# Optimization experiments

Hardware: AMD Instinct MI355X
Metric: run time of the kernel (lower is better)

The kernel has to match this reference:

```python
import jax, jax.numpy as jnp
import numpy as np

TEMPERATURE = 0.07
BASE_TEMPERATURE = 0.07


def _pairwise_euclid(x):
    # torch.cdist(x, x, p=2), with safe sqrt (zero grad at zero distance)
    sq = jnp.sum(x * x, axis=1)
    d2 = sq[:, None] + sq[None, :] - 2.0 * (x @ x.T)
    d2 = jnp.maximum(d2, 0.0)
    safe = jnp.where(d2 > 0.0, d2, 1.0)
    return jnp.where(d2 > 0.0, jnp.sqrt(safe), 0.0)


def setup_inputs() -> dict:
    key = jax.random.key(0)
    k1, k2 = jax.random.split(key)
    features = jax.random.normal(k1, (1024, 2, 512), dtype=jnp.float32)
    labels = jax.random.uniform(k2, (1024,), dtype=jnp.float32)
    return {"features": features, "labels": labels}


def reference(features, labels):
    B, V, D = features.shape
    N = B * V
    # torch.cat(torch.unbind(features, dim=1), dim=0): views stacked -> [N, D]
    cf = features.transpose(1, 0, 2).reshape(N, D)
    lab = jnp.tile(labels, V)  # label of row i is labels[i % B]

    dist = _pairwise_euclid(cf)              # [N, N]
    logits = -dist / TEMPERATURE
    eye = jnp.eye(N, dtype=logits.dtype)
    w = jnp.exp(logits) * (1.0 - eye)        # exp(logits) with l == i excluded

    dis = jnp.abs(lab[:, None] - lab[None, :])  # |y_i - y_j|, symmetric

    # negative[i, j] = sum_{l != i, |y_l - y_i| >= |y_i - y_j|} exp(logits[i, l])
    # computed per-row via sort + suffix cumsum + searchsorted (O(N^2 log N))
    order = jnp.argsort(dis, axis=1)
    sorted_d = jnp.take_along_axis(dis, order, axis=1)
    sorted_w = jnp.take_along_axis(w, order, axis=1)
    suffix = jnp.flip(jnp.cumsum(jnp.flip(sorted_w, axis=1), axis=1), axis=1)
    suffix = jnp.concatenate([suffix, jnp.zeros((N, 1), suffix.dtype)], axis=1)  # [N, N+1]
    # side='left': counts entries strictly < d, so suffix[idx] sums all >= d (ties incl.)
    idx = jax.vmap(lambda sd, d: jnp.searchsorted(sd, d, side='left'))(sorted_d, dis)
    negative = jnp.take_along_axis(suffix, idx, axis=1)
    negative = negative * (1.0 - eye) + eye  # diag set to 1 (log -> 0)

    logits_z = logits * (1.0 - eye)          # logits[i, i] = 0
    log_prob = logits_z - jnp.log(negative)
    mean_log_prob_pos = jnp.sum(log_prob, axis=1) / (N - 1)
    loss = -(TEMPERATURE / BASE_TEMPERATURE) * jnp.mean(mean_log_prob_pos)
    return loss
```

## Files before the change

### kernel.cpp

```cpp
#include <hip/hip_runtime.h>
#include <math.h>


#define NN 2048
#define BB 1024
#define DD 512
#define NT 256
#define NEGINF (-INFINITY)
#define CS 64.0f

typedef short s16x8 __attribute__((ext_vector_type(8)));
typedef float f32x4 __attribute__((ext_vector_type(4)));

__device__ __forceinline__ const float* cf_row(const float* F, int i) {
    return F + ((size_t)(i & (BB - 1)) * 2 + (size_t)(i >> 10)) * DD;
}

__device__ __forceinline__ unsigned bf_rne(float x) {
    const unsigned u = __float_as_uint(x);
    return (u + 0x7FFFu + ((u >> 16) & 1u)) >> 16;
}
__device__ __forceinline__ float bf_val(unsigned h) {
    return __uint_as_float(h << 16);
}

__global__ __launch_bounds__(512) void prep_sort_kernel(const float* __restrict__ F,
                                                        const float* __restrict__ labels,
                                                        ushort* __restrict__ Ahi,
                                                        ushort* __restrict__ Alo,
                                                        float* __restrict__ sq,
                                                        float* __restrict__ slab,
                                                        int* __restrict__ sj) {
    __shared__ float lab[BB];
    const int blk = blockIdx.x;
    const int t = threadIdx.x;

    if (blk < 256) {
        const int lane = t & 63;
        const int w = t >> 6;
        const int i = blk * 8 + w;
        const float* src = cf_row(F, i);
        const float4 v0 = reinterpret_cast<const float4*>(src)[lane];
        const float4 v1 = reinterpret_cast<const float4*>(src)[lane + 64];
        float ss = v0.x * v0.x + v0.y * v0.y + v0.z * v0.z + v0.w * v0.w
                 + v1.x * v1.x + v1.y * v1.y + v1.z * v1.z + v1.w * v1.w;
        #pragma unroll
        for (int st = 32; st > 0; st >>= 1) ss += __shfl_down(ss, st);
        if (lane == 0) sq[i] = ss;

        const float a[8] = {v0.x, v0.y, v0.z, v0.w, v1.x, v1.y, v1.z, v1.w};
        ushort h[8], l[8];
        #pragma unroll
        for (int e = 0; e < 8; ++e) {
            const unsigned hb = bf_rne(a[e]);
            h[e] = (ushort)hb;
            l[e] = (ushort)bf_rne(a[e] - bf_val(hb));
        }
        const size_t base = (size_t)i * DD;
        *reinterpret_cast<ushort4*>(&Ahi[base + lane * 4])       = make_ushort4(h[0], h[1], h[2], h[3]);
        *reinterpret_cast<ushort4*>(&Ahi[base + 256 + lane * 4]) = make_ushort4(h[4], h[5], h[6], h[7]);
        *reinterpret_cast<ushort4*>(&Alo[base + lane * 4])       = make_ushort4(l[0], l[1], l[2], l[3]);
        *reinterpret_cast<ushort4*>(&Alo[base + 256 + lane * 4]) = make_ushort4(l[4], l[5], l[6], l[7]);
    } else {
        lab[t] = labels[t];
        lab[t + 512] = labels[t + 512];
        __syncthreads();
        const int e = (blk - 256) * 512 + t;
        const float li = lab[e];
        int rank = 0;
        const float4* l4 = reinterpret_cast<const float4*>(lab);
        #pragma unroll 4
        for (int j = 0; j < BB / 4; ++j) {
            const float4 v = l4[j];
            const int j0 = j * 4;
            rank += (v.x < li) || (v.x == li && (j0 + 0) < e);
            rank += (v.y < li) || (v.y == li && (j0 + 1) < e);
            rank += (v.z < li) || (v.z == li && (j0 + 2) < e);
            rank += (v.w < li) || (v.w == li && (j0 + 3) < e);
        }
        slab[2 * rank]     = li;
        slab[2 * rank + 1] = li;
        sj[2 * rank]     = e;
        sj[2 * rank + 1] = e + BB;
    }
}

#define TM 64
#define TN 64
#define TK 32
__global__ __launch_bounds__(256) void gemm_dist_kernel(const ushort* __restrict__ Ahi,
                                                        const ushort* __restrict__ Alo,
                                                        const float* __restrict__ sq,
                                                        const int* __restrict__ sj,
                                                        float* __restrict__ distp) {
    __shared__ ushort Ah[4][TM][8];
    __shared__ ushort Al[4][TM][8];
    __shared__ ushort Bh[4][TN][8];
    __shared__ ushort Bl[4][TN][8];
    __shared__ int   sjcA[TM];
    __shared__ int   sjcB[TN];
    __shared__ float sqA[TM];
    __shared__ float sqB[TN];

    const int t = threadIdx.x;
    const int lane = t & 63;
    const int w = t >> 6;

    const int id = blockIdx.x;
    int by = (int)((__fsqrt_rn(8.0f * (float)id + 1.0f) - 1.0f) * 0.5f);
    while ((by + 1) * (by + 2) / 2 <= id) ++by;
    while (by * (by + 1) / 2 > id) --by;
    const int bx = id - by * (by + 1) / 2;
    const int row0 = by * TM;
    const int col0 = bx * TN;
    const bool below = (bx < by);

    if (t < TM) {
        const int s = sj[row0 + t];
        sjcA[t] = s; sqA[t] = sq[s];
    } else if (t < TM + TN) {
        const int u = t - TM;
        const int s = sj[col0 + u];
        sjcB[u] = s; sqB[u] = sq[s];
    }
    __syncthreads();
    const int rr = t >> 2;
    const int cq = t & 3;
    const size_t gA = (size_t)sjcA[rr] * DD + cq * 8;
    const size_t gB = (size_t)sjcB[rr] * DD + cq * 8;

    f32x4 acc[4] = {};
    const int m = lane & 15;
    const int q = lane >> 4;

    for (int kt = 0; kt < DD / TK; ++kt) {
        __syncthreads();
        const size_t ko = (size_t)kt * TK;
        *reinterpret_cast<int4*>(&Ah[cq][rr][0]) = *reinterpret_cast<const int4*>(&Ahi[gA + ko]);
        *reinterpret_cast<int4*>(&Al[cq][rr][0]) = *reinterpret_cast<const int4*>(&Alo[gA + ko]);
        *reinterpret_cast<int4*>(&Bh[cq][rr][0]) = *reinterpret_cast<const int4*>(&Ahi[gB + ko]);
        *reinterpret_cast<int4*>(&Bl[cq][rr][0]) = *reinterpret_cast<const int4*>(&Alo[gB + ko]);
        __syncthreads();

        const s16x8 fah = *reinterpret_cast<const s16x8*>(&Ah[q][w * 16 + m][0]);
        const s16x8 fal = *reinterpret_cast<const s16x8*>(&Al[q][w * 16 + m][0]);
        #pragma unroll
        for (int nt = 0; nt < 4; ++nt) {
            const s16x8 fbh = *reinterpret_cast<const s16x8*>(&Bh[q][nt * 16 + m][0]);
            const s16x8 fbl = *reinterpret_cast<const s16x8*>(&Bl[q][nt * 16 + m][0]);
            acc[nt] = __builtin_amdgcn_mfma_f32_16x16x32_bf16(fah, fbh, acc[nt], 0, 0, 0);
            acc[nt] = __builtin_amdgcn_mfma_f32_16x16x32_bf16(fah, fbl, acc[nt], 0, 0, 0);
            acc[nt] = __builtin_amdgcn_mfma_f32_16x16x32_bf16(fal, fbh, acc[nt], 0, 0, 0);
        }
    }

    const int lr0 = w * 16 + q * 4;
    #pragma unroll
    for (int nt = 0; nt < 4; ++nt) {
        const int lc = nt * 16 + m;
        float o[4];
        #pragma unroll
        for (int r = 0; r < 4; ++r) {
            const float d2 = sqA[lr0 + r] + sqB[lc] - 2.0f * acc[nt][r];
            o[r] = (d2 > 0.f) ? sqrtf(d2) : 0.f;
        }
        #pragma unroll
        for (int r = 0; r < 4; ++r)
            distp[(size_t)(row0 + lr0 + r) * NN + col0 + lc] = o[r];
        if (below) {
            const float4 o4 = make_float4(o[0], o[1], o[2], o[3]);
            *reinterpret_cast<float4*>(&distp[(size_t)(col0 + lc) * NN + row0 + lr0]) = o4;
        }
    }
}

__device__ __forceinline__ int bs_right(const float* key, float d, int lo, int hi) {
    while (lo < hi) {
        const int mid = (lo + hi) >> 1;
        if (key[mid] >= d) hi = mid; else lo = mid + 1;
    }
    return lo;
}
__device__ __forceinline__ int bs_left(const float* key, float d, int lo, int hi) {
    while (lo < hi) {
        const int mid = (lo + hi) >> 1;
        if (key[mid] < d) hi = mid; else lo = mid + 1;
    }
    return lo;
}

__global__ __launch_bounds__(512) void row_kernel(const float* __restrict__ distp,
                                                  const float* __restrict__ slab,
                                                  double* __restrict__ rowval) {
    __shared__ float key[NN];
    __shared__ float Pf[NN];
    __shared__ float Sf[NN + 1];
    __shared__ float wmxA[8], wmxB[8], wps[8], wss[8];
    __shared__ double wDA[8], wLA[8], wDB[8], wLB[8];

    const int pr = blockIdx.x;
    const int rA = 2 * pr, rB = 2 * pr + 1;
    const int t = threadIdx.x;
    const int lane = t & 63;
    const int w = t >> 6;
    const float x = slab[rA];
    const float negInvT = -1.0f / 0.07f;
    const float* drowA = &distp[(size_t)rA * NN];
    const float* drowB = &distp[(size_t)rB * NN];

    {
        const float4 l4 = reinterpret_cast<const float4*>(slab)[t];
        key[t * 4 + 0] = fabsf(l4.x - x);
        key[t * 4 + 1] = fabsf(l4.y - x);
        key[t * 4 + 2] = fabsf(l4.z - x);
        key[t * 4 + 3] = fabsf(l4.w - x);
    }
    const int cb = t * 4;
    float vA[4], vB[4];
    double dsumA = 0.0, dsumB = 0.0;
    float mxA = NEGINF, mxB = NEGINF;
    {
        const float4 a4 = reinterpret_cast<const float4*>(drowA)[t];
        const float4 b4 = reinterpret_cast<const float4*>(drowB)[t];
        const float av[4] = {a4.x, a4.y, a4.z, a4.w};
        const float bv[4] = {b4.x, b4.y, b4.z, b4.w};
        #pragma unroll
        for (int c = 0; c < 4; ++c) {
            const int pc = cb + c;
            if (pc == rA) vA[c] = NEGINF;
            else { const float vv = av[c] * negInvT; vA[c] = vv; mxA = fmaxf(mxA, vv); dsumA += (double)av[c]; }
            if (pc == rB) vB[c] = NEGINF;
            else { const float vv = bv[c] * negInvT; vB[c] = vv; mxB = fmaxf(mxB, vv); dsumB += (double)bv[c]; }
        }
    }
    #pragma unroll
    for (int st = 32; st > 0; st >>= 1) {
        mxA = fmaxf(mxA, __shfl_down(mxA, st));
        mxB = fmaxf(mxB, __shfl_down(mxB, st));
    }
    if (lane == 0) { wmxA[w] = mxA; wmxB[w] = mxB; }
    __syncthreads();
    const float MA = fmaxf(fmaxf(fmaxf(wmxA[0], wmxA[1]), fmaxf(wmxA[2], wmxA[3])),
                           fmaxf(fmaxf(wmxA[4], wmxA[5]), fmaxf(wmxA[6], wmxA[7])));
    const float MB = fmaxf(fmaxf(fmaxf(wmxB[0], wmxB[1]), fmaxf(wmxB[2], wmxB[3])),
                           fmaxf(fmaxf(wmxB[4], wmxB[5]), fmaxf(wmxB[6], wmxB[7])));

    int L8[4], R8[4];
    const int a = cb, b = cb + 3;
    {
        const int le = (rA - 1 < b) ? rA - 1 : b;
        if (a <= le) {
            const float da = key[a];
            const int Ra = bs_right(key, da, rA, NN);
            int Rl = Ra;
            if (le > a) Rl = bs_right(key, key[le], rA, Ra);
            for (int p = a; p <= le; ++p) {
                const float d = key[p];
                int R;
                if (p == a) R = Ra;
                else if (p == le) R = Rl;
                else R = bs_right(key, d, Rl, Ra);
                int L = p + 1;
                while (L < rA && key[L] == d) ++L;
                L8[p - a] = L; R8[p - a] = R;
            }
        }
        const int rs = (rA + 1 > a) ? rA + 1 : a;
        if (rs <= b) {
            const float dr = key[rs];
            const int Lr = bs_left(key, dr, 0, rA);
            int Lb = Lr;
            if (b > rs) Lb = bs_left(key, key[b], 0, Lr);
            for (int p = rs; p <= b; ++p) {
                const float d = key[p];
                int L;
                if (p == rs) L = Lr;
                else if (p == b) L = Lb;
                else L = bs_left(key, d, Lb, Lr);
                int R = p;
                while (R > rA && key[R - 1] == d) --R;
                L8[p - a] = L; R8[p - a] = R;
            }
        }
        if (rA >= a && rA <= b) { L8[rA - a] = rA; R8[rA - a] = rA; }
    }

    double lnsumA = 0.0;
    {
        float e8[4];
        #pragma unroll
        for (int jj = 0; jj < 4; ++jj) e8[jj] = __expf(vA[jj] - MA + CS);
        {
            float run = 0.f, ex[4];
            #pragma unroll
            for (int jj = 0; jj < 4; ++jj) { ex[jj] = run; run += e8[jj]; }
            float inc = run;
            #pragma unroll
            for (int st = 1; st < 64; st <<= 1) {
                const float nm = __shfl_up(inc, st);
                if (lane >= st) inc += nm;
            }
            float xofs = __shfl_up(inc, 1);
            if (lane == 0) xofs = 0.f;
            if (lane == 63) wps[w] = inc;
            __syncthreads();
            #pragma unroll
            for (int ww = 0; ww < 7; ++ww)
                if (ww < w) xofs += wps[ww];
            #pragma unroll
            for (int jj = 0; jj < 4; ++jj) Pf[cb + jj] = ex[jj] + xofs;
        }
        {
            float run = 0.f, sx[4];
            #pragma unroll
            for (int jj = 3; jj >= 0; --jj) { run += e8[jj]; sx[jj] = run; }
            float inc = run;
            #pragma unroll
            for (int st = 1; st < 64; st <<= 1) {
                const float nm = __shfl_down(inc, st);
                if (lane + st < 64) inc += nm;
            }
            float xofs = __shfl_down(inc, 1);
            if (lane == 63) xofs = 0.f;
            if (lane == 0) wss[w] = inc;
            __syncthreads();
            #pragma unroll
            for (int ww = 1; ww < 8; ++ww)
                if (ww > w) xofs += wss[ww];
            #pragma unroll
            for (int jj = 0; jj < 4; ++jj) Sf[cb + jj] = sx[jj] + xofs;
            if (t == 0) Sf[NN] = 0.f;
        }
        __syncthreads();
        const float MBA = MA - CS;
        #pragma unroll
        for (int jj = 0; jj < 4; ++jj) {
            const int p = cb + jj;
            if (p == rA) continue;
            const float s = fmaxf(Pf[L8[jj]] + Sf[R8[jj]], 1e-38f);
            lnsumA += (double)(MBA + __logf(s));
        }
    }
    __syncthreads();

    double lnsumB = 0.0;
    {
        float e8[4];
        #pragma unroll
        for (int jj = 0; jj < 4; ++jj) e8[jj] = __expf(vB[jj] - MB + CS);
        {
            float run = 0.f, ex[4];
            #pragma unroll
            for (int jj = 0; jj < 4; ++jj) { ex[jj] = run; run += e8[jj]; }
            float inc = run;
            #pragma unroll
            for (int st = 1; st < 64; st <<= 1) {
                const float nm = __shfl_up(inc, st);
                if (lane >= st) inc += nm;
            }
            float xofs = __shfl_up(inc, 1);
            if (lane == 0) xofs = 0.f;
            if (lane == 63) wps[w] = inc;
            __syncthreads();
            #pragma unroll
            for (int ww = 0; ww < 7; ++ww)
                if (ww < w) xofs += wps[ww];
            #pragma unroll
            for (int jj = 0; jj < 4; ++jj) Pf[cb + jj] = ex[jj] + xofs;
        }
        {
            float run = 0.f, sx[4];
            #pragma unroll
            for (int jj = 3; jj >= 0; --jj) { run += e8[jj]; sx[jj] = run; }
            float inc = run;
            #pragma unroll
            for (int st = 1; st < 64; st <<= 1) {
                const float nm = __shfl_down(inc, st);
                if (lane + st < 64) inc += nm;
            }
            float xofs = __shfl_down(inc, 1);
            if (lane == 63) xofs = 0.f;
            if (lane == 0) wss[w] = inc;
            __syncthreads();
            #pragma unroll
            for (int ww = 1; ww < 8; ++ww)
                if (ww > w) xofs += wss[ww];
            #pragma unroll
            for (int jj = 0; jj < 4; ++jj) Sf[cb + jj] = sx[jj] + xofs;
            if (t == 0) Sf[NN] = 0.f;
        }
        __syncthreads();
        const float MBB = MB - CS;
        #pragma unroll
        for (int jj = 0; jj < 4; ++jj) {
            const int p = cb + jj;
            if (p == rB) continue;
            const float s = fmaxf(Pf[L8[jj]] + Sf[R8[jj]], 1e-38f);
            lnsumB += (double)(MBB + __logf(s));
        }
    }

    #pragma unroll
    for (int st = 32; st > 0; st >>= 1) {
        dsumA  += __shfl_down(dsumA, st);
        lnsumA += __shfl_down(lnsumA, st);
        dsumB  += __shfl_down(dsumB, st);
        lnsumB += __shfl_down(lnsumB, st);
    }
    if (lane == 0) { wDA[w] = dsumA; wLA[w] = lnsumA; wDB[w] = dsumB; wLB[w] = lnsumB; }
    __syncthreads();
    if (t == 0) {
        double dA = 0.0, lA = 0.0, dB = 0.0, lB = 0.0;
        #pragma unroll
        for (int ww = 0; ww < 8; ++ww) { dA += wDA[ww]; lA += wLA[ww]; dB += wDB[ww]; lB += wLB[ww]; }
        rowval[rA] = (-dA / 0.07) - lA;
        rowval[rB] = (-dB / 0.07) - lB;
    }
}

__global__ __launch_bounds__(256) void finalize_kernel(const double* __restrict__ rowval,
                                                       float* __restrict__ out) {
    __shared__ double red[NT];
    const int t = threadIdx.x;
    double s = 0.0;
    for (int j = t; j < NN; j += NT) s += rowval[j];
    red[t] = s;
    __syncthreads();
    for (int ofs = NT / 2; ofs > 0; ofs >>= 1) {
        if (t < ofs) red[t] += red[t + ofs];
        __syncthreads();
    }
    if (t == 0) {
        out[0] = (float)(-red[0] / ((double)NN * (double)(NN - 1)));
    }
}

extern "C" void kernel_launch(void* const* d_in, const int* in_sizes, int n_in,
                              void* d_out, int out_size, void* d_ws, size_t ws_size,
                              hipStream_t stream) {
    const float* features = (const float*)d_in[0];
    const float* labels   = (const float*)d_in[1];
    float* out = (float*)d_out;

    char* ws = (char*)d_ws;
    size_t off = 0;
    float*  sq     = (float*) (ws + off); off += NN * sizeof(float);
    float*  slab   = (float*) (ws + off); off += NN * sizeof(float);
    int*    sj     = (int*)   (ws + off); off += NN * sizeof(int);
    double* rowval = (double*)(ws + off); off += NN * sizeof(double);
    ushort* Ahi    = (ushort*)(ws + off); off += (size_t)NN * DD * sizeof(ushort);
    ushort* Alo    = (ushort*)(ws + off); off += (size_t)NN * DD * sizeof(ushort);
    float*  distp  = (float*) (ws + off); off += (size_t)NN * NN * sizeof(float);

    prep_sort_kernel<<<258, 512, 0, stream>>>(features, labels, Ahi, Alo, sq, slab, sj);
    gemm_dist_kernel<<<528, NT, 0, stream>>>(Ahi, Alo, sq, sj, distp);
    row_kernel<<<NN / 2, 512, 0, stream>>>(distp, slab, rowval);
    finalize_kernel<<<1, NT, 0, stream>>>(rowval, out);
}
```

Before: 136.7 us.

## Double-buffer GEMM tiles via direct global-to-LDS loads and fuse final reduction

The GEMM main loop now stages K-tiles with global_load_lds into a double-buffered LDS array, prefetching the next tile while MFMAs run on the current one, with a single barrier per iteration. The separate finalize kernel is removed. Each row block instead atomically adds its pair value into a double accumulator, and the last block, detected by an atomic counter, writes the loss. This cuts one kernel launch and overlaps memory with compute, at the cost of nondeterministic summation order and reliance on correct async LDS load ordering.

```diff
diff --git a/kernel.cpp b/kernel.cpp
--- a/kernel.cpp
+++ b/kernel.cpp
@@ -24,13 +24,19 @@
     return __uint_as_float(h << 16);
 }
 
+#define GLOAD16(gp, lp) __builtin_amdgcn_global_load_lds( \
+    (const __attribute__((address_space(1))) void*)(gp),  \
+    (__attribute__((address_space(3))) void*)(lp), 16, 0, 0)
+
 __global__ __launch_bounds__(512) void prep_sort_kernel(const float* __restrict__ F,
                                                         const float* __restrict__ labels,
                                                         ushort* __restrict__ Ahi,
                                                         ushort* __restrict__ Alo,
                                                         float* __restrict__ sq,
                                                         float* __restrict__ slab,
-                                                        int* __restrict__ sj) {
+                                                        int* __restrict__ sj,
+                                                        double* __restrict__ accd,
+                                                        int* __restrict__ cnt) {
     __shared__ float lab[BB];
     const int blk = blockIdx.x;
     const int t = threadIdx.x;
@@ -62,6 +68,7 @@
         *reinterpret_cast<ushort4*>(&Alo[base + lane * 4])       = make_ushort4(l[0], l[1], l[2], l[3]);
         *reinterpret_cast<ushort4*>(&Alo[base + 256 + lane * 4]) = make_ushort4(l[4], l[5], l[6], l[7]);
     } else {
+        if (blk == 257 && t == 0) { *accd = 0.0; *cnt = 0; }
         lab[t] = labels[t];
         lab[t + 512] = labels[t + 512];
         __syncthreads();
@@ -88,15 +95,13 @@
 #define TM 64
 #define TN 64
 #define TK 32
+#define NKT (DD / TK)
 __global__ __launch_bounds__(256) void gemm_dist_kernel(const ushort* __restrict__ Ahi,
                                                         const ushort* __restrict__ Alo,
                                                         const float* __restrict__ sq,
                                                         const int* __restrict__ sj,
                                                         float* __restrict__ distp) {
-    __shared__ ushort Ah[4][TM][8];
-    __shared__ ushort Al[4][TM][8];
-    __shared__ ushort Bh[4][TN][8];
-    __shared__ ushort Bl[4][TN][8];
+    __shared__ __align__(16) ushort lds[2][4][4][64][8];
     __shared__ int   sjcA[TM];
     __shared__ int   sjcB[TN];
     __shared__ float sqA[TM];
@@ -124,34 +129,43 @@
         sjcB[u] = s; sqB[u] = sq[s];
     }
     __syncthreads();
-    const int rr = t >> 2;
-    const int cq = t & 3;
-    const size_t gA = (size_t)sjcA[rr] * DD + cq * 8;
-    const size_t gB = (size_t)sjcB[rr] * DD + cq * 8;
+
+    const ushort* gAh = Ahi + (size_t)sjcA[lane] * DD + w * 8;
+    const ushort* gAl = Alo + (size_t)sjcA[lane] * DD + w * 8;
+    const ushort* gBh = Ahi + (size_t)sjcB[lane] * DD + w * 8;
+    const ushort* gBl = Alo + (size_t)sjcB[lane] * DD + w * 8;
+
+#define STAGE(buf, kt) do {                                   \
+    const size_t ko_ = (size_t)(kt) * TK;                     \
+    GLOAD16(gAh + ko_, &lds[buf][0][w][0][0]);                \
+    GLOAD16(gAl + ko_, &lds[buf][1][w][0][0]);                \
+    GLOAD16(gBh + ko_, &lds[buf][2][w][0][0]);                \
+    GLOAD16(gBl + ko_, &lds[buf][3][w][0][0]);                \
+} while (0)
+
+    STAGE(0, 0);
+    __syncthreads();
 
     f32x4 acc[4] = {};
     const int m = lane & 15;
     const int q = lane >> 4;
 
-    for (int kt = 0; kt < DD / TK; ++kt) {
-        __syncthreads();
-        const size_t ko = (size_t)kt * TK;
-        *reinterpret_cast<int4*>(&Ah[cq][rr][0]) = *reinterpret_cast<const int4*>(&Ahi[gA + ko]);
-        *reinterpret_cast<int4*>(&Al[cq][rr][0]) = *reinterpret_cast<const int4*>(&Alo[gA + ko]);
-        *reinterpret_cast<int4*>(&Bh[cq][rr][0]) = *reinterpret_cast<const int4*>(&Ahi[gB + ko]);
-        *reinterpret_cast<int4*>(&Bl[cq][rr][0]) = *reinterpret_cast<const int4*>(&Alo[gB + ko]);
-        __syncthreads();
-
-        const s16x8 fah = *reinterpret_cast<const s16x8*>(&Ah[q][w * 16 + m][0]);
-        const s16x8 fal = *reinterpret_cast<const s16x8*>(&Al[q][w * 16 + m][0]);
+    for (int kt = 0; kt < NKT; ++kt) {
+        const int cur = kt & 1;
+        if (kt + 1 < NKT) {
+            if (cur) STAGE(0, kt + 1); else STAGE(1, kt + 1);
+        }
+        const s16x8 fah = *reinterpret_cast<const s16x8*>(&lds[cur][0][q][w * 16 + m][0]);
+        const s16x8 fal = *reinterpret_cast<const s16x8*>(&lds[cur][1][q][w * 16 + m][0]);
         #pragma unroll
         for (int nt = 0; nt < 4; ++nt) {
-            const s16x8 fbh = *reinterpret_cast<const s16x8*>(&Bh[q][nt * 16 + m][0]);
-            const s16x8 fbl = *reinterpret_cast<const s16x8*>(&Bl[q][nt * 16 + m][0]);
+            const s16x8 fbh = *reinterpret_cast<const s16x8*>(&lds[cur][2][q][nt * 16 + m][0]);
+            const s16x8 fbl = *reinterpret_cast<const s16x8*>(&lds[cur][3][q][nt * 16 + m][0]);
             acc[nt] = __builtin_amdgcn_mfma_f32_16x16x32_bf16(fah, fbh, acc[nt], 0, 0, 0);
             acc[nt] = __builtin_amdgcn_mfma_f32_16x16x32_bf16(fah, fbl, acc[nt], 0, 0, 0);
             acc[nt] = __builtin_amdgcn_mfma_f32_16x16x32_bf16(fal, fbh, acc[nt], 0, 0, 0);
         }
+        __syncthreads();
     }
 
     const int lr0 = w * 16 + q * 4;
@@ -172,6 +186,7 @@
             *reinterpret_cast<float4*>(&distp[(size_t)(col0 + lc) * NN + row0 + lr0]) = o4;
         }
     }
+#undef STAGE
 }
 
 __device__ __forceinline__ int bs_right(const float* key, float d, int lo, int hi) {
@@ -191,7 +206,9 @@
 
 __global__ __launch_bounds__(512) void row_kernel(const float* __restrict__ distp,
                                                   const float* __restrict__ slab,
-                                                  double* __restrict__ rowval) {
+                                                  double* __restrict__ accd,
+                                                  int* __restrict__ cnt,
+                                                  float* __restrict__ out) {
     __shared__ float key[NN];
     __shared__ float Pf[NN];
     __shared__ float Sf[NN + 1];
@@ -413,25 +430,15 @@
         double dA = 0.0, lA = 0.0, dB = 0.0, lB = 0.0;
         #pragma unroll
         for (int ww = 0; ww < 8; ++ww) { dA += wDA[ww]; lA += wLA[ww]; dB += wDB[ww]; lB += wLB[ww]; }
-        rowval[rA] = (-dA / 0.07) - lA;
-        rowval[rB] = (-dB / 0.07) - lB;
-    }
-}
-
-__global__ __launch_bounds__(256) void finalize_kernel(const double* __restrict__ rowval,
-                                                       float* __restrict__ out) {
-    __shared__ double red[NT];
-    const int t = threadIdx.x;
-    double s = 0.0;
-    for (int j = t; j < NN; j += NT) s += rowval[j];
-    red[t] = s;
-    __syncthreads();
-    for (int ofs = NT / 2; ofs > 0; ofs >>= 1) {
-        if (t < ofs) red[t] += red[t + ofs];
-        __syncthreads();
-    }
-    if (t == 0) {
-        out[0] = (float)(-red[0] / ((double)NN * (double)(NN - 1)));
+        const double pairv = ((-dA / 0.07) - lA) + ((-dB / 0.07) - lB);
+        atomicAdd(accd, pairv);
+        __threadfence();
+        const int old = atomicAdd(cnt, 1);
+        if (old == NN / 2 - 1) {
+            __threadfence();
+            const double tot = atomicAdd(accd, 0.0);
+            out[0] = (float)(-tot / ((double)NN * (double)(NN - 1)));
+        }
     }
 }
 
@@ -447,13 +454,13 @@
     float*  sq     = (float*) (ws + off); off += NN * sizeof(float);
     float*  slab   = (float*) (ws + off); off += NN * sizeof(float);
     int*    sj     = (int*)   (ws + off); off += NN * sizeof(int);
-    double* rowval = (double*)(ws + off); off += NN * sizeof(double);
+    double* accd   = (double*)(ws + off); off += sizeof(double);
+    int*    cnt    = (int*)   (ws + off); off += 2 * sizeof(int);
     ushort* Ahi    = (ushort*)(ws + off); off += (size_t)NN * DD * sizeof(ushort);
     ushort* Alo    = (ushort*)(ws + off); off += (size_t)NN * DD * sizeof(ushort);
     float*  distp  = (float*) (ws + off); off += (size_t)NN * NN * sizeof(float);
 
-    prep_sort_kernel<<<258, 512, 0, stream>>>(features, labels, Ahi, Alo, sq, slab, sj);
+    prep_sort_kernel<<<258, 512, 0, stream>>>(features, labels, Ahi, Alo, sq, slab, sj, accd, cnt);
     gemm_dist_kernel<<<528, NT, 0, stream>>>(Ahi, Alo, sq, sj, distp);
-    row_kernel<<<NN / 2, 512, 0, stream>>>(distp, slab, rowval);
-    finalize_kernel<<<1, NT, 0, stream>>>(rowval, out);
-}
+    row_kernel<<<NN / 2, 512, 0, stream>>>(distp, slab, accd, cnt, out);
+}
```

New measurement: 159.3 us. 1.17x slower.
